# Kernel tuning notes

Measured on AMD Instinct MI355X. Metric: run time of the kernel, lower is better.

The kernel has to match this reference:

```python
import jax, jax.numpy as jnp
import numpy as np

N = 6144
F_IN, H1, H2, EMB = 512, 256, 128, 64
ALPHA = 0.2  # LeakyReLU negative slope
NEG_INF = -9e15


def setup_inputs() -> dict:
    key = jax.random.key(0)
    ks = jax.random.split(key, 12)
    x = jax.random.normal(ks[0], (N, F_IN), dtype=jnp.float32)
    adj = (jax.random.uniform(ks[1], (N, N)) < 0.01).astype(jnp.float32)
    adj = jnp.maximum(adj, jnp.eye(N, dtype=jnp.float32))
    M = jax.random.uniform(ks[2], (N, N), dtype=jnp.float32)

    def glorot(k, shape):
        lim = float(np.sqrt(6.0 / (shape[0] + shape[1])))
        return jax.random.uniform(k, shape, jnp.float32, -lim, lim)

    params = {
        "W1": glorot(ks[3], (F_IN, H1)), "a_s1": glorot(ks[4], (H1, 1)), "a_n1": glorot(ks[5], (H1, 1)),
        "W2": glorot(ks[6], (H1, H2)),  "a_s2": glorot(ks[7], (H2, 1)), "a_n2": glorot(ks[8], (H2, 1)),
        "W3": glorot(ks[9], (H2, EMB)), "a_s3": glorot(ks[10], (EMB, 1)), "a_n3": glorot(ks[11], (EMB, 1)),
    }
    return {"x": x, "adj": adj, "M": M, **params}


def _gat_layer(x, adj, M, W, a_s, a_n):
    h = x @ W                                   # [N, d_out]
    e = (h @ a_s) + (h @ a_n).T                 # [N, N] pairwise logits
    e = jax.nn.leaky_relu(e * M, ALPHA)
    e = jnp.where(adj > 0, e, NEG_INF)
    att = jax.nn.softmax(e, axis=1)             # masked row softmax
    return jax.nn.elu(att @ h)


def reference(x, adj, M, W1, a_s1, a_n1, W2, a_s2, a_n2, W3, a_s3, a_n3):
    h = _gat_layer(x, adj, M, W1, a_s1, a_n1)
    h = _gat_layer(h, adj, M, W2, a_s2, a_n2)
    h = _gat_layer(h, adj, M, W3, a_s3, a_n3)
    z = h / jnp.maximum(jnp.linalg.norm(h, axis=1, keepdims=True), 1e-12)
    A_pred = jax.nn.sigmoid(z @ z.T)
    return (A_pred, z)
```

## Files before the change

kernel.cpp:

```cpp
#include <hip/hip_runtime.h>
#include <hip/hip_bf16.h>
#include <math.h>

#define NROW 6144
#define LRELU_ALPHA 0.2f
#define MAXD 128

typedef __attribute__((ext_vector_type(8))) __bf16 bf16x8;
typedef __attribute__((ext_vector_type(16))) float f32x16;

__global__ __launch_bounds__(256) void prep_scan(
    const float* __restrict__ adj, uint32_t* __restrict__ bm,
    const float* __restrict__ W1, const float* __restrict__ W2, const float* __restrict__ W3,
    __bf16* __restrict__ w1h, __bf16* __restrict__ w1l,
    __bf16* __restrict__ w2h, __bf16* __restrict__ w2l,
    __bf16* __restrict__ w3h, __bf16* __restrict__ w3l,
    const float* __restrict__ as1, const float* __restrict__ an1,
    const float* __restrict__ as2, const float* __restrict__ an2,
    const float* __restrict__ as3, const float* __restrict__ an3,
    float* __restrict__ wsa1, float* __restrict__ wna1,
    float* __restrict__ wsa2, float* __restrict__ wna2,
    float* __restrict__ wsa3, float* __restrict__ wna3) {
  int b = blockIdx.x;
  if (b < NROW) {
    const int id = b * 256 + threadIdx.x;
    const int row = id >> 8, sub = id & 255;
    const float4* ap = (const float4*)(adj + (size_t)row * NROW) + (sub >> 6) * 384 + (sub & 63);
    uint32_t mk = 0;
#pragma unroll
    for (int it = 0; it < 6; ++it) {
      float4 a = ap[it * 64];
      uint32_t q = (uint32_t)(a.x > 0.f) | ((uint32_t)(a.y > 0.f) << 1) |
                   ((uint32_t)(a.z > 0.f) << 2) | ((uint32_t)(a.w > 0.f) << 3);
      mk |= q << (it * 4);
    }
    bm[id] = mk;
    return;
  }
  b -= NROW;
  if (b < 672) {
    int idx = b * 256 + threadIdx.x;
    const float* W; __bf16 *wh, *wl; int K, D;
    if (idx < 131072) { W = W1; wh = w1h; wl = w1l; K = 512; D = 256; }
    else if (idx < 163840) { idx -= 131072; W = W2; wh = w2h; wl = w2l; K = 256; D = 128; }
    else { idx -= 163840; if (idx >= 8192) return; W = W3; wh = w3h; wl = w3l; K = 128; D = 64; }
    int k = idx / D, d = idx - k * D;
    float v = W[idx];
    __bf16 h = (__bf16)v;
    wh[(size_t)d * K + k] = h;
    wl[(size_t)d * K + k] = (__bf16)(v - (float)h);
    return;
  }
  int t = (b - 672) * 256 + threadIdx.x;
  if (t < 512) {
    float s = 0.f, n = 0.f;
    for (int d = 0; d < 256; ++d) { float w = W1[t * 256 + d]; s = fmaf(w, as1[d], s); n = fmaf(w, an1[d], n); }
    wsa1[t] = s; wna1[t] = n;
  } else if (t < 768) {
    int k = t - 512;
    float s = 0.f, n = 0.f;
    for (int d = 0; d < 128; ++d) { float w = W2[k * 128 + d]; s = fmaf(w, as2[d], s); n = fmaf(w, an2[d], n); }
    wsa2[k] = s; wna2[k] = n;
  } else if (t < 896) {
    int k = t - 768;
    float s = 0.f, n = 0.f;
    for (int d = 0; d < 64; ++d) { float w = W3[k * 64 + d]; s = fmaf(w, as3[d], s); n = fmaf(w, an3[d], n); }
    wsa3[k] = s; wna3[k] = n;
  }
}

__global__ __launch_bounds__(256) void csr_from_bitmap(const uint32_t* __restrict__ bm,
                                                       const float* __restrict__ Mm,
                                                       int* __restrict__ cnt,
                                                       int* __restrict__ cidx,
                                                       float* __restrict__ cmval) {
  const int row = blockIdx.x;
  const int tid = threadIdx.x, wv = tid >> 6, lane = tid & 63;
  __shared__ int wtot[4];
  __shared__ int jsh[MAXD];
  const uint32_t mask = bm[row * 256 + tid];
  const int pc = __popc(mask);
  int pre = pc;
#pragma unroll
  for (int off = 1; off < 64; off <<= 1) {
    int t = __shfl_up(pre, off);
    if (lane >= off) pre += t;
  }
  if (lane == 63) wtot[wv] = pre;
  __syncthreads();
  int base = pre - pc;
  for (int w = 0; w < wv; ++w) base += wtot[w];
  const int total = min(wtot[0] + wtot[1] + wtot[2] + wtot[3], MAXD);
  uint32_t m = mask;
  int p = base;
  const int cb0 = wv * 1536 + lane * 4;
  while (m) {
    int bit = __ffs(m) - 1;
    m &= m - 1;
    if (p < MAXD) jsh[p] = cb0 + ((bit >> 2) << 8) + (bit & 3);
    ++p;
  }
  __syncthreads();
  const float* mrow = Mm + (size_t)row * NROW;
  for (int k = tid; k < total; k += 256) {
    int j = jsh[k];
    cidx[(size_t)row * MAXD + k] = j;
    cmval[(size_t)row * MAXD + k] = mrow[j];
  }
  if (tid == 0) cnt[row] = total;
}

template <int SPLIT>
__global__ __launch_bounds__(256) void gemm_lsk(
    const float* __restrict__ A,
    const __bf16* __restrict__ Bth, const __bf16* __restrict__ Btl,
    const float* __restrict__ wsa, const float* __restrict__ wna,
    float* __restrict__ sv, float* __restrict__ nv,
    float* __restrict__ C, __bf16* __restrict__ Cb, int K, int D) {
  __shared__ float accs[SPLIT - 1][16][64];
  __shared__ float svs[SPLIT][32], nvs[SPLIT][32];
  const int wv = threadIdx.x >> 6, lane = threadIdx.x & 63;
  const int l31 = lane & 31, lh = lane >> 5;
  const int ib = blockIdx.x * 32, jb = blockIdx.y * 32;
  const int KC = K / SPLIT, k0 = wv * KC;
  const float* Arow = A + (size_t)(ib + l31) * K + lh * 8;
  const __bf16* Bh = Bth + (size_t)(jb + l31) * K + lh * 8;
  const __bf16* Bl = Btl + (size_t)(jb + l31) * K + lh * 8;
  const bool do_sn = (blockIdx.y == 0);
  f32x16 acc;
#pragma unroll
  for (int r = 0; r < 16; ++r) acc[r] = 0.f;
  float ss = 0.f, nn = 0.f;
  for (int k = k0; k < k0 + KC; k += 16) {
    float4 a0 = *(const float4*)(Arow + k);
    float4 a1 = *(const float4*)(Arow + k + 4);
    bf16x8 bh = *(const bf16x8*)(Bh + k);
    bf16x8 bl = *(const bf16x8*)(Bl + k);
    float av[8] = {a0.x, a0.y, a0.z, a0.w, a1.x, a1.y, a1.z, a1.w};
    if (do_sn) {
      float4 s0 = *(const float4*)(wsa + k + lh * 8);
      float4 s1 = *(const float4*)(wsa + k + lh * 8 + 4);
      float4 n0 = *(const float4*)(wna + k + lh * 8);
      float4 n1 = *(const float4*)(wna + k + lh * 8 + 4);
      ss = fmaf(av[0], s0.x, ss); ss = fmaf(av[1], s0.y, ss);
      ss = fmaf(av[2], s0.z, ss); ss = fmaf(av[3], s0.w, ss);
      ss = fmaf(av[4], s1.x, ss); ss = fmaf(av[5], s1.y, ss);
      ss = fmaf(av[6], s1.z, ss); ss = fmaf(av[7], s1.w, ss);
      nn = fmaf(av[0], n0.x, nn); nn = fmaf(av[1], n0.y, nn);
      nn = fmaf(av[2], n0.z, nn); nn = fmaf(av[3], n0.w, nn);
      nn = fmaf(av[4], n1.x, nn); nn = fmaf(av[5], n1.y, nn);
      nn = fmaf(av[6], n1.z, nn); nn = fmaf(av[7], n1.w, nn);
    }
    bf16x8 ah, al;
#pragma unroll
    for (int t = 0; t < 8; ++t) {
      __bf16 h = (__bf16)av[t];
      ah[t] = h;
      al[t] = (__bf16)(av[t] - (float)h);
    }
    acc = __builtin_amdgcn_mfma_f32_32x32x16_bf16(ah, bh, acc, 0, 0, 0);
    acc = __builtin_amdgcn_mfma_f32_32x32x16_bf16(ah, bl, acc, 0, 0, 0);
    acc = __builtin_amdgcn_mfma_f32_32x32x16_bf16(al, bh, acc, 0, 0, 0);
  }
  if (do_sn) {
    ss += __shfl_xor(ss, 32);
    nn += __shfl_xor(nn, 32);
    if (lh == 0) { svs[wv][l31] = ss; nvs[wv][l31] = nn; }
  }
  if (wv > 0) {
#pragma unroll
    for (int r = 0; r < 16; ++r) accs[wv - 1][r][lane] = acc[r];
  }
  __syncthreads();
  if (wv == 0) {
#pragma unroll
    for (int w = 0; w < SPLIT - 1; ++w)
#pragma unroll
      for (int r = 0; r < 16; ++r) acc[r] += accs[w][r][lane];
    if (do_sn && lh == 0) {
      float s = 0.f, n = 0.f;
#pragma unroll
      for (int w = 0; w < SPLIT; ++w) { s += svs[w][l31]; n += nvs[w][l31]; }
      sv[ib + l31] = s;
      nv[ib + l31] = n;
    }
#pragma unroll
    for (int r = 0; r < 16; ++r) {
      int rowi = (r & 3) + 8 * (r >> 2) + 4 * lh;
      if (C)  C[(size_t)(ib + rowi) * D + jb + l31] = acc[r];
      if (Cb) Cb[(size_t)(ib + rowi) * D + jb + l31] = (__bf16)acc[r];
    }
  }
}

template <int D, int WPR, bool BF16G, bool NORM>
__global__ __launch_bounds__(256) void attn_csr(const float* __restrict__ h,
                                                const __bf16* __restrict__ hb,
                                                const int* __restrict__ cnt,
                                                const int* __restrict__ cidx,
                                                const float* __restrict__ cmval,
                                                const float* __restrict__ sv,
                                                const float* __restrict__ nv,
                                                float* __restrict__ out,
                                                __bf16* __restrict__ zb) {
  constexpr int RPB = 4 / WPR;
  constexpr int CW = D / WPR;
  constexpr int NQ = BF16G ? 2 : CW / 64;
  __shared__ float ws[4][MAXD];
  __shared__ int js[4][MAXD];
  const int wv = threadIdx.x >> 6, lane = threadIdx.x & 63;
  const int row = blockIdx.x * RPB + wv / WPR;
  const int half = wv % WPR;
  const int c = cnt[row];
  const float si = sv[row];
  const size_t cb = (size_t)row * MAXD;

  float e0 = -1e30f, e1 = -1e30f;
  int j0 = 0, j1 = 0;
  if (lane < c) {
    j0 = cidx[cb + lane];
    float v = (si + nv[j0]) * cmval[cb + lane];
    e0 = v > 0.f ? v : LRELU_ALPHA * v;
  }
  if (lane + 64 < c) {
    j1 = cidx[cb + lane + 64];
    float v = (si + nv[j1]) * cmval[cb + lane + 64];
    e1 = v > 0.f ? v : LRELU_ALPHA * v;
  }
  float mx = fmaxf(e0, e1);
#pragma unroll
  for (int off = 32; off; off >>= 1) mx = fmaxf(mx, __shfl_xor(mx, off));
  float w0 = lane < c ? __expf(e0 - mx) : 0.f;
  float w1 = lane + 64 < c ? __expf(e1 - mx) : 0.f;
  float s = w0 + w1;
#pragma unroll
  for (int off = 32; off; off >>= 1) s += __shfl_xor(s, off);
  const float inv = 1.f / s;
  ws[wv][lane] = w0 * inv;
  ws[wv][lane + 64] = w1 * inv;
  js[wv][lane] = j0;
  js[wv][lane + 64] = j1;
  const int cbase = half * CW;
  float acc[NQ];
#pragma unroll
  for (int q = 0; q < NQ; ++q) acc[q] = 0.f;
  if (BF16G) {
#pragma unroll 8
    for (int k = 0; k < c; ++k) {
      const float wk = ws[wv][k];
      const uint32_t* hr = (const uint32_t*)(hb + (size_t)js[wv][k] * D + cbase);
      uint32_t v = hr[lane];
      acc[0] = fmaf(wk, __uint_as_float(v << 16), acc[0]);
      acc[1] = fmaf(wk, __uint_as_float(v & 0xffff0000u), acc[1]);
    }
    float2 o;
    o.x = acc[0] > 0.f ? acc[0] : expm1f(acc[0]);
    o.y = acc[1] > 0.f ? acc[1] : expm1f(acc[1]);
    *(float2*)(out + (size_t)row * D + cbase + lane * 2) = o;
  } else {
#pragma unroll 8
    for (int k = 0; k < c; ++k) {
      const float wk = ws[wv][k];
      const float* hr = h + (size_t)js[wv][k] * D + cbase;
#pragma unroll
      for (int q = 0; q < NQ; ++q) acc[q] = fmaf(wk, hr[lane + q * 64], acc[q]);
    }
    if (!NORM) {
#pragma unroll
      for (int q = 0; q < NQ; ++q) {
        float a = acc[q];
        out[(size_t)row * D + cbase + lane + q * 64] = a > 0.f ? a : expm1f(a);
      }
    } else {
      float a = acc[0];
      a = a > 0.f ? a : expm1f(a);
      float sq = a * a;
#pragma unroll
      for (int off = 32; off; off >>= 1) sq += __shfl_xor(sq, off);
      float zv = a / fmaxf(sqrtf(sq), 1e-12f);
      out[(size_t)row * 64 + lane] = zv;
      zb[(size_t)row * 64 + lane] = (__bf16)zv;
    }
  }
}

__global__ __launch_bounds__(256) void decoder_mfma(const __bf16* __restrict__ zb,
                                                    float* __restrict__ out) {
  const int wv = threadIdx.x >> 6, lane = threadIdx.x & 63;
  const int ib = blockIdx.y * 64 + (wv >> 1) * 32;
  const int jb = blockIdx.x * 64 + (wv & 1) * 32;
  const int l31 = lane & 31, lh = lane >> 5;
  const __bf16* Arow = zb + (size_t)(ib + l31) * 64 + lh * 8;
  const __bf16* Brow = zb + (size_t)(jb + l31) * 64 + lh * 8;
  f32x16 acc;
#pragma unroll
  for (int r = 0; r < 16; ++r) acc[r] = 0.f;
#pragma unroll
  for (int kk = 0; kk < 4; ++kk) {
    bf16x8 af = *(const bf16x8*)(Arow + kk * 16);
    bf16x8 bfv = *(const bf16x8*)(Brow + kk * 16);
    acc = __builtin_amdgcn_mfma_f32_32x32x16_bf16(af, bfv, acc, 0, 0, 0);
  }
#pragma unroll
  for (int r = 0; r < 16; ++r) {
    int rowi = (r & 3) + 8 * (r >> 2) + 4 * lh;
    float v = 1.f / (1.f + __expf(-acc[r]));
    out[(size_t)(ib + rowi) * NROW + jb + l31] = v;
  }
}

extern "C" void kernel_launch(void* const* d_in, const int* in_sizes, int n_in,
                              void* d_out, int out_size, void* d_ws, size_t ws_size,
                              hipStream_t stream) {
  const float* x   = (const float*)d_in[0];
  const float* adj = (const float*)d_in[1];
  const float* Mm  = (const float*)d_in[2];
  const float* W1  = (const float*)d_in[3];
  const float* as1 = (const float*)d_in[4];
  const float* an1 = (const float*)d_in[5];
  const float* W2  = (const float*)d_in[6];
  const float* as2 = (const float*)d_in[7];
  const float* an2 = (const float*)d_in[8];
  const float* W3  = (const float*)d_in[9];
  const float* as3 = (const float*)d_in[10];
  const float* an3 = (const float*)d_in[11];

  float* out = (float*)d_out;
  float* z = out + (size_t)NROW * NROW;

  float* wsp = (float*)d_ws;
  float* hA   = wsp;
  float* hB   = hA + (size_t)NROW * 256;
  float* sv   = hB + (size_t)NROW * 256;
  float* nv   = sv + NROW;
  float* cmv  = nv + NROW;
  int*   cix  = (int*)(cmv + (size_t)NROW * MAXD);
  int*   cct  = cix + (size_t)NROW * MAXD;
  __bf16* zb  = (__bf16*)(cct + NROW);
  __bf16* w1h = zb + (size_t)NROW * 64;
  __bf16* w1l = w1h + 512 * 256;
  __bf16* w2h = w1l + 512 * 256;
  __bf16* w2l = w2h + 256 * 128;
  __bf16* w3h = w2l + 256 * 128;
  __bf16* w3l = w3h + 128 * 64;
  float* wsa1 = (float*)(w3l + 128 * 64);
  float* wna1 = wsa1 + 512;
  float* wsa2 = wna1 + 512;
  float* wna2 = wsa2 + 256;
  float* wsa3 = wna2 + 256;
  float* wna3 = wsa3 + 128;
  __bf16* hAb = (__bf16*)(wna3 + 128);
  uint32_t* bmp = (uint32_t*)(hAb + (size_t)NROW * 256);

  dim3 b256(256);

  prep_scan<<<dim3(NROW + 676), b256, 0, stream>>>(
      adj, bmp, W1, W2, W3, w1h, w1l, w2h, w2l, w3h, w3l,
      as1, an1, as2, an2, as3, an3, wsa1, wna1, wsa2, wna2, wsa3, wna3);

  csr_from_bitmap<<<dim3(NROW), b256, 0, stream>>>(bmp, Mm, cct, cix, cmv);

  gemm_lsk<4><<<dim3(NROW / 32, 256 / 32), b256, 0, stream>>>(x, w1h, w1l, wsa1, wna1, sv, nv, nullptr, hAb, 512, 256);
  attn_csr<256, 2, true, false><<<dim3(NROW / 2), b256, 0, stream>>>(nullptr, hAb, cct, cix, cmv, sv, nv, hB, nullptr);

  gemm_lsk<4><<<dim3(NROW / 32, 128 / 32), b256, 0, stream>>>(hB, w2h, w2l, wsa2, wna2, sv, nv, nullptr, hAb, 256, 128);
  attn_csr<128, 1, true, false><<<dim3(NROW / 4), b256, 0, stream>>>(nullptr, hAb, cct, cix, cmv, sv, nv, hB, nullptr);

  gemm_lsk<4><<<dim3(NROW / 32, 64 / 32), b256, 0, stream>>>(hB, w3h, w3l, wsa3, wna3, sv, nv, hA, nullptr, 128, 64);
  attn_csr<64, 1, false, true><<<dim3(NROW / 4), b256, 0, stream>>>(hA, nullptr, cct, cix, cmv, sv, nv, z, zb);

  decoder_mfma<<<dim3(NROW / 64, NROW / 64), b256, 0, stream>>>(zb, out);
}
```

Baseline: 187.6 us.

## Replace split-K register GEMM with LDS-tiled 64x64 block GEMM

```diff
diff --git a/kernel.cpp b/kernel.cpp
--- a/kernel.cpp
+++ b/kernel.cpp
@@ -110,86 +110,77 @@
   if (tid == 0) cnt[row] = total;
 }
 
-template <int SPLIT>
-__global__ __launch_bounds__(256) void gemm_lsk(
+__global__ __launch_bounds__(256) void gemm_lds(
     const float* __restrict__ A,
     const __bf16* __restrict__ Bth, const __bf16* __restrict__ Btl,
     const float* __restrict__ wsa, const float* __restrict__ wna,
     float* __restrict__ sv, float* __restrict__ nv,
     float* __restrict__ C, __bf16* __restrict__ Cb, int K, int D) {
-  __shared__ float accs[SPLIT - 1][16][64];
-  __shared__ float svs[SPLIT][32], nvs[SPLIT][32];
-  const int wv = threadIdx.x >> 6, lane = threadIdx.x & 63;
+  __shared__ __bf16 Ah[64][72], Al[64][72], Bh[64][72], Bl[64][72];
+  const int tid = threadIdx.x;
+  const int wv = tid >> 6, lane = tid & 63;
   const int l31 = lane & 31, lh = lane >> 5;
-  const int ib = blockIdx.x * 32, jb = blockIdx.y * 32;
-  const int KC = K / SPLIT, k0 = wv * KC;
-  const float* Arow = A + (size_t)(ib + l31) * K + lh * 8;
-  const __bf16* Bh = Bth + (size_t)(jb + l31) * K + lh * 8;
-  const __bf16* Bl = Btl + (size_t)(jb + l31) * K + lh * 8;
-  const bool do_sn = (blockIdx.y == 0);
+  const int wr = wv >> 1, wc = wv & 1;
+  const int rb = blockIdx.x * 64, jb = blockIdx.y * 64;
+  const bool do_sn = (blockIdx.y == 0) && (wc == 0);
   f32x16 acc;
 #pragma unroll
   for (int r = 0; r < 16; ++r) acc[r] = 0.f;
   float ss = 0.f, nn = 0.f;
-  for (int k = k0; k < k0 + KC; k += 16) {
-    float4 a0 = *(const float4*)(Arow + k);
-    float4 a1 = *(const float4*)(Arow + k + 4);
-    bf16x8 bh = *(const bf16x8*)(Bh + k);
-    bf16x8 bl = *(const bf16x8*)(Bl + k);
-    float av[8] = {a0.x, a0.y, a0.z, a0.w, a1.x, a1.y, a1.z, a1.w};
-    if (do_sn) {
-      float4 s0 = *(const float4*)(wsa + k + lh * 8);
-      float4 s1 = *(const float4*)(wsa + k + lh * 8 + 4);
-      float4 n0 = *(const float4*)(wna + k + lh * 8);
-      float4 n1 = *(const float4*)(wna + k + lh * 8 + 4);
-      ss = fmaf(av[0], s0.x, ss); ss = fmaf(av[1], s0.y, ss);
-      ss = fmaf(av[2], s0.z, ss); ss = fmaf(av[3], s0.w, ss);
-      ss = fmaf(av[4], s1.x, ss); ss = fmaf(av[5], s1.y, ss);
-      ss = fmaf(av[6], s1.z, ss); ss = fmaf(av[7], s1.w, ss);
-      nn = fmaf(av[0], n0.x, nn); nn = fmaf(av[1], n0.y, nn);
-      nn = fmaf(av[2], n0.z, nn); nn = fmaf(av[3], n0.w, nn);
-      nn = fmaf(av[4], n1.x, nn); nn = fmaf(av[5], n1.y, nn);
-      nn = fmaf(av[6], n1.z, nn); nn = fmaf(av[7], n1.w, nn);
-    }
-    bf16x8 ah, al;
-#pragma unroll
-    for (int t = 0; t < 8; ++t) {
-      __bf16 h = (__bf16)av[t];
-      ah[t] = h;
-      al[t] = (__bf16)(av[t] - (float)h);
-    }
-    acc = __builtin_amdgcn_mfma_f32_32x32x16_bf16(ah, bh, acc, 0, 0, 0);
-    acc = __builtin_amdgcn_mfma_f32_32x32x16_bf16(ah, bl, acc, 0, 0, 0);
-    acc = __builtin_amdgcn_mfma_f32_32x32x16_bf16(al, bh, acc, 0, 0, 0);
+  for (int kt = 0; kt < K; kt += 64) {
+#pragma unroll
+    for (int c2 = 0; c2 < 4; ++c2) {
+      int flat = c2 * 256 + tid;
+      int row = flat >> 4, cq = (flat & 15) * 4;
+      float4 a = *(const float4*)(A + (size_t)(rb + row) * K + kt + cq);
+      __bf16 h0 = (__bf16)a.x, h1 = (__bf16)a.y, h2 = (__bf16)a.z, h3 = (__bf16)a.w;
+      Ah[row][cq] = h0; Ah[row][cq + 1] = h1; Ah[row][cq + 2] = h2; Ah[row][cq + 3] = h3;
+      Al[row][cq] = (__bf16)(a.x - (float)h0);
+      Al[row][cq + 1] = (__bf16)(a.y - (float)h1);
+      Al[row][cq + 2] = (__bf16)(a.z - (float)h2);
+      Al[row][cq + 3] = (__bf16)(a.w - (float)h3);
+    }
+#pragma unroll
+    for (int c2 = 0; c2 < 2; ++c2) {
+      int flat = c2 * 256 + tid;
+      int row = flat >> 3, cq = (flat & 7) * 8;
+      *(bf16x8*)&Bh[row][cq] = *(const bf16x8*)(Bth + (size_t)(jb + row) * K + kt + cq);
+      *(bf16x8*)&Bl[row][cq] = *(const bf16x8*)(Btl + (size_t)(jb + row) * K + kt + cq);
+    }
+    __syncthreads();
+#pragma unroll
+    for (int kk = 0; kk < 4; ++kk) {
+      bf16x8 af  = *(const bf16x8*)&Ah[wr * 32 + l31][kk * 16 + lh * 8];
+      bf16x8 alf = *(const bf16x8*)&Al[wr * 32 + l31][kk * 16 + lh * 8];
+      bf16x8 bhf = *(const bf16x8*)&Bh[wc * 32 + l31][kk * 16 + lh * 8];
+      bf16x8 blf = *(const bf16x8*)&Bl[wc * 32 + l31][kk * 16 + lh * 8];
+      if (do_sn) {
+        const float* wsp = wsa + kt + kk * 16 + lh * 8;
+        const float* wnp = wna + kt + kk * 16 + lh * 8;
+#pragma unroll
+        for (int t = 0; t < 8; ++t) {
+          float av = (float)af[t] + (float)alf[t];
+          ss = fmaf(av, wsp[t], ss);
+          nn = fmaf(av, wnp[t], nn);
+        }
+      }
+      acc = __builtin_amdgcn_mfma_f32_32x32x16_bf16(af, bhf, acc, 0, 0, 0);
+      acc = __builtin_amdgcn_mfma_f32_32x32x16_bf16(af, blf, acc, 0, 0, 0);
+      acc = __builtin_amdgcn_mfma_f32_32x32x16_bf16(alf, bhf, acc, 0, 0, 0);
+    }
+    __syncthreads();
   }
   if (do_sn) {
     ss += __shfl_xor(ss, 32);
     nn += __shfl_xor(nn, 32);
-    if (lh == 0) { svs[wv][l31] = ss; nvs[wv][l31] = nn; }
-  }
-  if (wv > 0) {
-#pragma unroll
-    for (int r = 0; r < 16; ++r) accs[wv - 1][r][lane] = acc[r];
-  }
-  __syncthreads();
-  if (wv == 0) {
-#pragma unroll
-    for (int w = 0; w < SPLIT - 1; ++w)
-#pragma unroll
-      for (int r = 0; r < 16; ++r) acc[r] += accs[w][r][lane];
-    if (do_sn && lh == 0) {
-      float s = 0.f, n = 0.f;
-#pragma unroll
-      for (int w = 0; w < SPLIT; ++w) { s += svs[w][l31]; n += nvs[w][l31]; }
-      sv[ib + l31] = s;
-      nv[ib + l31] = n;
-    }
-#pragma unroll
-    for (int r = 0; r < 16; ++r) {
-      int rowi = (r & 3) + 8 * (r >> 2) + 4 * lh;
-      if (C)  C[(size_t)(ib + rowi) * D + jb + l31] = acc[r];
-      if (Cb) Cb[(size_t)(ib + rowi) * D + jb + l31] = (__bf16)acc[r];
-    }
+    if (lh == 0) { sv[rb + wr * 32 + l31] = ss; nv[rb + wr * 32 + l31] = nn; }
+  }
+#pragma unroll
+  for (int r = 0; r < 16; ++r) {
+    int rowi = (r & 3) + 8 * (r >> 2) + 4 * lh + wr * 32;
+    int col = jb + wc * 32 + l31;
+    if (C)  C[(size_t)(rb + rowi) * D + col] = acc[r];
+    if (Cb) Cb[(size_t)(rb + rowi) * D + col] = (__bf16)acc[r];
   }
 }
 
@@ -360,13 +351,13 @@
 
   csr_from_bitmap<<<dim3(NROW), b256, 0, stream>>>(bmp, Mm, cct, cix, cmv);
 
-  gemm_lsk<4><<<dim3(NROW / 32, 256 / 32), b256, 0, stream>>>(x, w1h, w1l, wsa1, wna1, sv, nv, nullptr, hAb, 512, 256);
+  gemm_lds<<<dim3(NROW / 64, 256 / 64), b256, 0, stream>>>(x, w1h, w1l, wsa1, wna1, sv, nv, nullptr, hAb, 512, 256);
   attn_csr<256, 2, true, false><<<dim3(NROW / 2), b256, 0, stream>>>(nullptr, hAb, cct, cix, cmv, sv, nv, hB, nullptr);
 
-  gemm_lsk<4><<<dim3(NROW / 32, 128 / 32), b256, 0, stream>>>(hB, w2h, w2l, wsa2, wna2, sv, nv, nullptr, hAb, 256, 128);
+  gemm_lds<<<dim3(NROW / 64, 128 / 64), b256, 0, stream>>>(hB, w2h, w2l, wsa2, wna2, sv, nv, nullptr, hAb, 256, 128);
   attn_csr<128, 1, true, false><<<dim3(NROW / 4), b256, 0, stream>>>(nullptr, hAb, cct, cix, cmv, sv, nv, hB, nullptr);
 
-  gemm_lsk<4><<<dim3(NROW / 32, 64 / 32), b256, 0, stream>>>(hB, w3h, w3l, wsa3, wna3, sv, nv, hA, nullptr, 128, 64);
+  gemm_lds<<<dim3(NROW / 64, 64 / 64), b256, 0, stream>>>(hB, w3h, w3l, wsa3, wna3, sv, nv, hA, nullptr, 128, 64);
   attn_csr<64, 1, false, true><<<dim3(NROW / 4), b256, 0, stream>>>(hA, nullptr, cct, cix, cmv, sv, nv, z, zb);
 
   decoder_mfma<<<dim3(NROW / 64, NROW / 64), b256, 0, stream>>>(zb, out);
```

After: 175.0 us. -6.7%, faster.
